# Optimization experiments

Measured on AMD Instinct MI355X. Metric: run time of the kernel, lower is better.

The kernel has to match this reference:

```python
import jax, jax.numpy as jnp
import numpy as np

CHANNEL = 1
ALPHA = 1.0
EPS = 1e-10
SHAPE = (1, CHANNEL, 160, 192, 160)


def _sobel_kernels(channel):
    s2 = np.array([[-1., 0., 1.], [-2., 0., 2.], [-1., 0., 1.]], dtype=np.float32)
    # sobel.repeat(channel,1,3,1,1): 2D kernel tiled along depth -> k[d,h,w] = s2[h,w]
    kx = np.tile(s2[None, :, :], (3, 1, 1))
    ky = np.tile(s2.T[None, :, :], (3, 1, 1))
    kz = np.array([[[-1., -1., -1.], [-2., -2., -2.], [-1., -1., -1.]],
                   [[0., 0., 0.], [0., 0., 0.], [0., 0., 0.]],
                   [[1., 1., 1.], [2., 2., 2.], [1., 1., 1.]]], dtype=np.float32)
    def rep(k):  # -> [channel, 1, 3, 3, 3] for depthwise conv
        return jnp.asarray(np.tile(k[None, None], (channel, 1, 1, 1, 1)))
    return rep(kx), rep(ky), rep(kz)


def _conv3d(x, k, channel):
    # torch F.conv3d (cross-correlation), padding=1, groups=channel
    return jax.lax.conv_general_dilated(
        x, k, window_strides=(1, 1, 1), padding=((1, 1), (1, 1), (1, 1)),
        dimension_numbers=('NCDHW', 'OIDHW', 'NCDHW'),
        feature_group_count=channel)


def setup_inputs() -> dict:
    key = jax.random.key(0)
    k1, k2, k3 = jax.random.split(key, 3)
    M = jax.random.normal(k1, SHAPE, dtype=jnp.float32)
    S = jax.random.normal(k2, SHAPE, dtype=jnp.float32)
    flow = jax.random.normal(k3, (SHAPE[0], 3) + SHAPE[2:], dtype=jnp.float32)
    return {"M": M, "S": S, "flow": flow}


def reference(M, S, flow):
    kx, ky, kz = _sobel_kernels(CHANNEL)
    Idiff = M - S
    Sx = _conv3d(S, kx, CHANNEL)
    Sy = _conv3d(S, ky, CHANNEL)
    Sz = _conv3d(S, kz, CHANNEL)
    Mx = _conv3d(M, kx, CHANNEL)
    My = _conv3d(M, ky, CHANNEL)
    Mz = _conv3d(M, kz, CHANNEL)
    Sxyz_mag = Sx ** 2 + Sy ** 2 + Sz ** 2
    Mxyz_mag = Mx ** 2 + My ** 2 + Mz ** 2
    denom_S = Sxyz_mag + (ALPHA ** 2) * Idiff ** 2 + 1e-10
    denom_M = Mxyz_mag + (ALPHA ** 2) * Idiff ** 2 + 1e-10
    Ux = Idiff * (Sx / denom_S + Mx / denom_M)
    Uy = Idiff * (Sy / denom_S + My / denom_M)
    Uz = Idiff * (Sz / denom_S + Mz / denom_M)
    demons_ori_xz = jnp.arctan(Ux / (Uz + EPS))
    demons_ori_yz = jnp.arctan(Uy / (Uz + EPS))
    flow_ori_xz = jnp.arctan(flow[:, 0] / (flow[:, 2] + EPS))
    flow_ori_yz = jnp.arctan(flow[:, 1] / (flow[:, 2] + EPS))
    ori_error = jnp.mean((flow_ori_xz - demons_ori_xz) ** 2) + \
                jnp.mean((flow_ori_yz - demons_ori_yz) ** 2)
    return ori_error
```

## Files before the change

### kernel.cpp

```cpp
#include <hip/hip_runtime.h>
#include <math.h>

#define DD 160
#define HH 192
#define WW 160
#define TW 32
#define THB 16
#define TD 4
#define HW (HH * WW)
#define NVOX (DD * HW)
#define HTW 34
#define HTH 18
#define LSTR 34
#define HALO (HTH * HTW)

typedef float v2f __attribute__((ext_vector_type(2)));

__device__ __forceinline__ v2f vrcp(v2f a) {
    v2f r;
    r.x = __builtin_amdgcn_rcpf(a.x);
    r.y = __builtin_amdgcn_rcpf(a.y);
    return r;
}

__device__ __forceinline__ v2f atan_ratio(v2f num, v2f den) {
    v2f a = __builtin_elementwise_abs(num);
    v2f b = __builtin_elementwise_abs(den);
    v2f mn = __builtin_elementwise_min(a, b);
    v2f mx = __builtin_elementwise_max(a, b);
    v2f x = mn * vrcp(mx);
    v2f x2 = x * x;
    v2f p = __builtin_elementwise_fma(x2,
            __builtin_elementwise_fma(x2,
            __builtin_elementwise_fma(x2,
            __builtin_elementwise_fma(x2,
            __builtin_elementwise_fma(x2, (v2f)(-0.0117212f), (v2f)(0.05265332f)),
            (v2f)(-0.11643287f)), (v2f)(0.19354346f)), (v2f)(-0.33262347f)),
            (v2f)(0.99997726f));
    p *= x;
    v2f q = 1.57079632679489662f - p;
    v2f res;
    res.x = a.x > b.x ? q.x : p.x;
    res.y = a.y > b.y ? q.y : p.y;
    unsigned sx = (__float_as_uint(num.x) ^ __float_as_uint(den.x)) & 0x80000000u;
    unsigned sy = (__float_as_uint(num.y) ^ __float_as_uint(den.y)) & 0x80000000u;
    res.x = __uint_as_float(__float_as_uint(res.x) | sx);
    res.y = __uint_as_float(__float_as_uint(res.y) | sy);
    return res;
}

__global__ __launch_bounds__(256) void demons_ori_kernel(
    const float* __restrict__ Mv, const float* __restrict__ Sv,
    const float* __restrict__ flow, float* __restrict__ out)
{
    __shared__ float buf[2][2][HTH * LSTR];
    __shared__ float redbuf[4];

    const int tid = threadIdx.x;
    const int lane = tid & 63;
    const int wid = tid >> 6;
    const int tw = lane & 31;
    const int r  = wid * 4 + (lane >> 5) * 2;
    const int w0 = blockIdx.x * TW;
    const int h0 = blockIdx.y * THB;
    const int d0 = blockIdx.z * TD;

    const bool has2 = (tid < HALO - 512);
    int gb0, gb1, gb2 = 0;
    bool ok0, ok1, ok2 = false;
    {
        int i = tid;
        int hh = i / HTW, ww = i - HTW * hh;
        int gh = h0 + hh - 1, gw = w0 + ww - 1;
        ok0 = (gh >= 0 && gh < HH && gw >= 0 && gw < WW);
        gb0 = gh * WW + gw;
        i = tid + 256;
        hh = i / HTW; ww = i - HTW * hh;
        gh = h0 + hh - 1; gw = w0 + ww - 1;
        ok1 = (gh >= 0 && gh < HH && gw >= 0 && gw < WW);
        gb1 = gh * WW + gw;
        if (has2) {
            i = tid + 512;
            hh = i / HTW; ww = i - HTW * hh;
            gh = h0 + hh - 1; gw = w0 + ww - 1;
            ok2 = (gh >= 0 && gh < HH && gw >= 0 && gw < WW);
            gb2 = gh * WW + gw;
        }
    }

    float pS0 = 0.f, pM0 = 0.f, pS1 = 0.f, pM1 = 0.f, pS2 = 0.f, pM2 = 0.f;

    auto issue = [&](int d) {
        const bool din = (d >= 0) && (d < DD);
        const size_t base = (size_t)d * HW;
        pS0 = (din && ok0) ? Sv[base + gb0] : 0.f;
        pM0 = (din && ok0) ? Mv[base + gb0] : 0.f;
        pS1 = (din && ok1) ? Sv[base + gb1] : 0.f;
        pM1 = (din && ok1) ? Mv[base + gb1] : 0.f;
        pS2 = (din && ok2) ? Sv[base + gb2] : 0.f;
        pM2 = (din && ok2) ? Mv[base + gb2] : 0.f;
    };
    auto commit = [&](int d) {
        float* __restrict__ bS = &buf[d & 1][0][0];
        float* __restrict__ bM = &buf[d & 1][1][0];
        bS[tid] = pS0;        bM[tid] = pM0;
        bS[tid + 256] = pS1;  bM[tid + 256] = pM1;
        if (has2) { bS[tid + 512] = pS2; bM[tid + 512] = pM2; }
    };

    const int rb = r * LSTR + tw;
    auto fieldPartials = [&](const float* __restrict__ b,
                             v2f& Px, v2f& Py, v2f& Bq, v2f& Cq) {
        const float* r0 = b + rb;
        const float* r1 = r0 + LSTR;
        const float* r2 = r1 + LSTR;
        const float* r3 = r2 + LSTR;
        float a0 = r0[0], b0 = r0[1], c0 = r0[2];
        float a1 = r1[0], b1 = r1[1], c1 = r1[2];
        float a2 = r2[0], b2 = r2[1], c2 = r2[2];
        float a3 = r3[0], b3 = r3[1], c3 = r3[2];
        float X0 = c0 - a0, X1 = c1 - a1, X2 = c2 - a2, X3 = c3 - a3;
        float W0 = a0 + 2.f * b0 + c0, W1 = a1 + 2.f * b1 + c1;
        float W2 = a2 + 2.f * b2 + c2, W3 = a3 + 2.f * b3 + c3;
        float I0 = a0 + b0 + c0, I1 = a1 + b1 + c1;
        float I2 = a2 + b2 + c2, I3 = a3 + b3 + c3;
        Px = (v2f){X0 + 2.f * X1 + X2, X1 + 2.f * X2 + X3};
        Py = (v2f){W2 - W0, W3 - W1};
        Bq = (v2f){I0 + 2.f * I1 + I2, I1 + 2.f * I2 + I3};
        Cq = (v2f){b1, b2};
    };

    v2f mSPx, mSPy, mSB, mSC, mMPx, mMPy, mMB, mMC;
    v2f zSPx, zSPy, zSB, zSC, zMPx, zMPy, zMB, zMC;
    v2f pSPx, pSPy, pSB, pSC, pMPx, pMPy, pMB, pMC;

    issue(d0 - 1);
    commit(d0 - 1);
    issue(d0);
    __syncthreads();
    fieldPartials(&buf[(d0 - 1) & 1][0][0], mSPx, mSPy, mSB, mSC);
    fieldPartials(&buf[(d0 - 1) & 1][1][0], mMPx, mMPy, mMB, mMC);
    commit(d0);
    issue(d0 + 1);
    __syncthreads();
    fieldPartials(&buf[d0 & 1][0][0], zSPx, zSPy, zSB, zSC);
    fieldPartials(&buf[d0 & 1][1][0], zMPx, zMPy, zMB, zMC);

    const size_t voffA = (size_t)(h0 + r) * WW + (w0 + tw);
    v2f fFx, fFy, fFz;
    {
        size_t o = (size_t)d0 * HW + voffA;
        fFx = (v2f){flow[o], flow[o + WW]};
        fFy = (v2f){flow[NVOX + o], flow[NVOX + o + WW]};
        fFz = (v2f){flow[2 * (size_t)NVOX + o], flow[2 * (size_t)NVOX + o + WW]};
    }

    v2f vsum = (v2f){0.f, 0.f};

    #pragma unroll
    for (int dd = 0; dd < TD; ++dd) {
        const int d = d0 + dd;
        commit(d + 1);
        v2f nFx = (v2f){0.f, 0.f}, nFy = nFx, nFz = nFx;
        if (dd < TD - 1) {
            issue(d + 2);
            size_t o = (size_t)(d + 1) * HW + voffA;
            nFx = (v2f){flow[o], flow[o + WW]};
            nFy = (v2f){flow[NVOX + o], flow[NVOX + o + WW]};
            nFz = (v2f){flow[2 * (size_t)NVOX + o], flow[2 * (size_t)NVOX + o + WW]};
        }
        __syncthreads();
        fieldPartials(&buf[(d + 1) & 1][0][0], pSPx, pSPy, pSB, pSC);
        fieldPartials(&buf[(d + 1) & 1][1][0], pMPx, pMPy, pMB, pMC);

        v2f idf = zMC - zSC;
        v2f i2  = __builtin_elementwise_fma(idf, idf, (v2f)(1e-10f));
        v2f gxS = mSPx + zSPx + pSPx;
        v2f gyS = mSPy + zSPy + pSPy;
        v2f gzS = pSB - mSB;
        v2f gxM = mMPx + zMPx + pMPx;
        v2f gyM = mMPy + zMPy + pMPy;
        v2f gzM = pMB - mMB;
        v2f denS = __builtin_elementwise_fma(gxS, gxS,
                   __builtin_elementwise_fma(gyS, gyS,
                   __builtin_elementwise_fma(gzS, gzS, i2)));
        v2f denM = __builtin_elementwise_fma(gxM, gxM,
                   __builtin_elementwise_fma(gyM, gyM,
                   __builtin_elementwise_fma(gzM, gzM, i2)));
        v2f rS = vrcp(denS);
        v2f rM = vrcp(denM);
        v2f Ux = idf * __builtin_elementwise_fma(gxS, rS, gxM * rM);
        v2f Uy = idf * __builtin_elementwise_fma(gyS, rS, gyM * rM);
        v2f Uz = idf * __builtin_elementwise_fma(gzS, rS, gzM * rM);

        v2f uzp = Uz + 1e-10f;
        v2f dxz = atan_ratio(Ux, uzp);
        v2f dyz = atan_ratio(Uy, uzp);

        v2f fzp = fFz + 1e-10f;
        v2f fxz = atan_ratio(fFx, fzp);
        v2f fyz = atan_ratio(fFy, fzp);

        v2f e1 = fxz - dxz;
        v2f e2 = fyz - dyz;
        vsum = __builtin_elementwise_fma(e1, e1,
               __builtin_elementwise_fma(e2, e2, vsum));

        mSPx = zSPx; mSPy = zSPy; mSB = zSB; mSC = zSC;
        mMPx = zMPx; mMPy = zMPy; mMB = zMB; mMC = zMC;
        zSPx = pSPx; zSPy = pSPy; zSB = pSB; zSC = pSC;
        zMPx = pMPx; zMPy = pMPy; zMB = pMB; zMC = pMC;
        fFx = nFx; fFy = nFy; fFz = nFz;
    }

    float lsum = vsum.x + vsum.y;
    #pragma unroll
    for (int o = 32; o > 0; o >>= 1)
        lsum += __shfl_down(lsum, o, 64);
    if (lane == 0)
        redbuf[wid] = lsum;
    __syncthreads();
    if (tid == 0) {
        float s = redbuf[0] + redbuf[1] + redbuf[2] + redbuf[3];
        atomicAdd(out, s * (1.0f / (float)NVOX));
    }
}

extern "C" void kernel_launch(void* const* d_in, const int* in_sizes, int n_in,
                              void* d_out, int out_size, void* d_ws, size_t ws_size,
                              hipStream_t stream) {
    const float* Mv   = (const float*)d_in[0];
    const float* Sv   = (const float*)d_in[1];
    const float* flow = (const float*)d_in[2];
    float* out = (float*)d_out;

    hipMemsetAsync(out, 0, sizeof(float), stream);

    dim3 grid(WW / TW, HH / THB, DD / TD);
    demons_ori_kernel<<<grid, dim3(256), 0, stream>>>(Mv, Sv, flow, out);
}
```

Before: 139.8 us.

## Switch to horizontal 2-voxel thread mapping and deepen depth tile

After: 129.5 us. -7.4%, faster.

```diff
diff --git a/kernel.cpp b/kernel.cpp
--- a/kernel.cpp
+++ b/kernel.cpp
@@ -6,7 +6,7 @@
 #define WW 160
 #define TW 32
 #define THB 16
-#define TD 4
+#define TD 8
 #define HW (HH * WW)
 #define NVOX (DD * HW)
 #define HTW 34
@@ -59,8 +59,9 @@
     const int tid = threadIdx.x;
     const int lane = tid & 63;
     const int wid = tid >> 6;
-    const int tw = lane & 31;
-    const int r  = wid * 4 + (lane >> 5) * 2;
+    const int i16 = lane & 15;
+    const int r   = wid * 4 + (lane >> 4);
+    const int tw2 = 2 * i16;
     const int w0 = blockIdx.x * TW;
     const int h0 = blockIdx.y * THB;
     const int d0 = blockIdx.z * TD;
@@ -108,26 +109,27 @@
         if (has2) { bS[tid + 512] = pS2; bM[tid + 512] = pM2; }
     };
 
-    const int rb = r * LSTR + tw;
+    const int rb = r * LSTR + tw2;
     auto fieldPartials = [&](const float* __restrict__ b,
                              v2f& Px, v2f& Py, v2f& Bq, v2f& Cq) {
-        const float* r0 = b + rb;
-        const float* r1 = r0 + LSTR;
-        const float* r2 = r1 + LSTR;
-        const float* r3 = r2 + LSTR;
-        float a0 = r0[0], b0 = r0[1], c0 = r0[2];
-        float a1 = r1[0], b1 = r1[1], c1 = r1[2];
-        float a2 = r2[0], b2 = r2[1], c2 = r2[2];
-        float a3 = r3[0], b3 = r3[1], c3 = r3[2];
-        float X0 = c0 - a0, X1 = c1 - a1, X2 = c2 - a2, X3 = c3 - a3;
-        float W0 = a0 + 2.f * b0 + c0, W1 = a1 + 2.f * b1 + c1;
-        float W2 = a2 + 2.f * b2 + c2, W3 = a3 + 2.f * b3 + c3;
-        float I0 = a0 + b0 + c0, I1 = a1 + b1 + c1;
-        float I2 = a2 + b2 + c2, I3 = a3 + b3 + c3;
-        Px = (v2f){X0 + 2.f * X1 + X2, X1 + 2.f * X2 + X3};
-        Py = (v2f){W2 - W0, W3 - W1};
-        Bq = (v2f){I0 + 2.f * I1 + I2, I1 + 2.f * I2 + I3};
-        Cq = (v2f){b1, b2};
+        const float* p0 = b + rb;
+        const float* p1 = p0 + LSTR;
+        const float* p2 = p1 + LSTR;
+        v2f lo0 = *(const v2f*)p0, hi0 = *(const v2f*)(p0 + 2);
+        v2f lo1 = *(const v2f*)p1, hi1 = *(const v2f*)(p1 + 2);
+        v2f lo2 = *(const v2f*)p2, hi2 = *(const v2f*)(p2 + 2);
+        v2f X0 = hi0 - lo0, X1 = hi1 - lo1, X2 = hi2 - lo2;
+        v2f m0 = (v2f){lo0.y, hi0.x};
+        v2f m1 = (v2f){lo1.y, hi1.x};
+        v2f m2 = (v2f){lo2.y, hi2.x};
+        v2f s0 = lo0 + hi0, s1 = lo1 + hi1, s2 = lo2 + hi2;
+        v2f W0 = __builtin_elementwise_fma(m0, (v2f)(2.f), s0);
+        v2f W2 = __builtin_elementwise_fma(m2, (v2f)(2.f), s2);
+        v2f I0 = s0 + m0, I1 = s1 + m1, I2 = s2 + m2;
+        Px = __builtin_elementwise_fma(X1, (v2f)(2.f), X0) + X2;
+        Py = W2 - W0;
+        Bq = __builtin_elementwise_fma(I1, (v2f)(2.f), I0) + I2;
+        Cq = m1;
     };
 
     v2f mSPx, mSPy, mSB, mSC, mMPx, mMPy, mMB, mMC;
@@ -146,13 +148,13 @@
     fieldPartials(&buf[d0 & 1][0][0], zSPx, zSPy, zSB, zSC);
     fieldPartials(&buf[d0 & 1][1][0], zMPx, zMPy, zMB, zMC);
 
-    const size_t voffA = (size_t)(h0 + r) * WW + (w0 + tw);
+    const size_t voffA = (size_t)(h0 + r) * WW + (w0 + tw2);
     v2f fFx, fFy, fFz;
     {
         size_t o = (size_t)d0 * HW + voffA;
-        fFx = (v2f){flow[o], flow[o + WW]};
-        fFy = (v2f){flow[NVOX + o], flow[NVOX + o + WW]};
-        fFz = (v2f){flow[2 * (size_t)NVOX + o], flow[2 * (size_t)NVOX + o + WW]};
+        fFx = *(const v2f*)(flow + o);
+        fFy = *(const v2f*)(flow + NVOX + o);
+        fFz = *(const v2f*)(flow + 2 * (size_t)NVOX + o);
     }
 
     v2f vsum = (v2f){0.f, 0.f};
@@ -165,9 +167,9 @@
         if (dd < TD - 1) {
             issue(d + 2);
             size_t o = (size_t)(d + 1) * HW + voffA;
-            nFx = (v2f){flow[o], flow[o + WW]};
-            nFy = (v2f){flow[NVOX + o], flow[NVOX + o + WW]};
-            nFz = (v2f){flow[2 * (size_t)NVOX + o], flow[2 * (size_t)NVOX + o + WW]};
+            nFx = *(const v2f*)(flow + o);
+            nFy = *(const v2f*)(flow + NVOX + o);
+            nFz = *(const v2f*)(flow + 2 * (size_t)NVOX + o);
         }
         __syncthreads();
         fieldPartials(&buf[(d + 1) & 1][0][0], pSPx, pSPy, pSB, pSC);
```
